# Kernel optimization log

Measured on AMD Instinct MI355X. Metric: run time of the kernel, lower is better.

The kernel has to match this reference:

```python
import jax, jax.numpy as jnp
import numpy as np

N, E, D, H, C = 50000, 800000, 128, 4, 32  # nodes, edges, in/out dim, heads, head dim
NEG_SLOPE = 0.2
LN_EPS = 1e-5
NORM_EPS = 1e-12


def setup_inputs() -> dict:
    key = jax.random.key(0)
    ks = jax.random.split(key, 10)
    s = 1.0 / np.sqrt(D)
    return {
        "x": jax.random.normal(ks[0], (N, D), dtype=jnp.float32),
        "edge_index": jax.random.randint(ks[1], (2, E), 0, N, dtype=jnp.int64),
        "gamma": 1.0 + 0.1 * jax.random.normal(ks[2], (D,), dtype=jnp.float32),
        "beta": 0.1 * jax.random.normal(ks[3], (D,), dtype=jnp.float32),
        "W_l": jax.random.normal(ks[4], (D, H * C), dtype=jnp.float32) * s,
        "b_l": jnp.zeros((H * C,), dtype=jnp.float32),
        "W_r": jax.random.normal(ks[5], (D, H * C), dtype=jnp.float32) * s,
        "b_r": jnp.zeros((H * C,), dtype=jnp.float32),
        "att": jax.random.normal(ks[6], (H, C), dtype=jnp.float32) * s,
        "bias": jnp.zeros((H * C,), dtype=jnp.float32),
        "scale": jnp.array(1.0, dtype=jnp.float32),
    }


def reference(x, edge_index, gamma, beta, W_l, b_l, W_r, b_r, att, bias, scale):
    n = x.shape[0]
    # Pre-activation: LayerNorm -> ReLU (dropout=0 in eval)
    mu = jnp.mean(x, axis=-1, keepdims=True)
    var = jnp.mean(jnp.square(x - mu), axis=-1, keepdims=True)
    h = jax.nn.relu((x - mu) / jnp.sqrt(var + LN_EPS) * gamma + beta)

    # GATv2Conv (PyG defaults: add_self_loops=True, negative_slope=0.2)
    loops = jnp.arange(n, dtype=edge_index.dtype)
    src = jnp.concatenate([edge_index[0], loops])  # message source j
    dst = jnp.concatenate([edge_index[1], loops])  # message target i

    xl = (h @ W_l + b_l).reshape(n, H, C)
    xr = (h @ W_r + b_r).reshape(n, H, C)

    # per-edge GATv2 score: a^T LeakyReLU(xl[j] + xr[i])  -> [E2, H]
    feat = jax.nn.leaky_relu(xl[src] + xr[dst], NEG_SLOPE)
    e = jnp.einsum('ehc,hc->eh', feat, att)

    # segment softmax over incoming edges of each target node
    m = jax.ops.segment_max(e, dst, num_segments=n)
    p = jnp.exp(e - m[dst])
    denom = jax.ops.segment_sum(p, dst, num_segments=n)
    alpha = p / denom[dst]  # [E2, H]

    # scatter-aggregate weighted source features
    msg = alpha[:, :, None] * xl[src]  # [E2, H, C]
    out = jax.ops.segment_sum(msg, dst, num_segments=n).reshape(n, H * C) + bias

    # MsgNorm: normalize(msg) * ||h||_2 * scale
    out_norm = jnp.sqrt(jnp.sum(jnp.square(out), axis=-1, keepdims=True))
    msg_n = out / jnp.maximum(out_norm, NORM_EPS)
    h_norm = jnp.sqrt(jnp.sum(jnp.square(h), axis=-1, keepdims=True))
    gat_out = msg_n * h_norm * scale

    # residual (projection is None since in_channels == out_channels)
    return x + gat_out
```

## Files before the change

### kernel.cpp

```cpp
#include <hip/hip_runtime.h>
#include <hip/hip_bf16.h>
#include <math.h>

#define N_NODES 50000
#define N_EDGES 800000
#define E2 (N_EDGES + N_NODES)
#define D 128

#define NB_LN 12500
#define NB_W 128

#define BSHIFT 8
#define NBUCK 196
#define SCHUNK 4096
#define NB_SC ((E2 + SCHUNK - 1) / SCHUNK)
#define NB_GEMM (((N_NODES + 127) / 128) * 2)

typedef short short8 __attribute__((ext_vector_type(8)));
typedef float f32x4 __attribute__((ext_vector_type(4)));
typedef _Float16 h16x2 __attribute__((ext_vector_type(2)));
typedef _Float16 h16x8 __attribute__((ext_vector_type(8)));

__device__ __forceinline__ float waveReduceSum(float v) {
#pragma unroll
  for (int off = 32; off >= 1; off >>= 1) v += __shfl_xor(v, off);
  return v;
}

__device__ __forceinline__ h16x2 shfl_xor_h2(h16x2 v, int off) {
  int r = __shfl_xor(__builtin_bit_cast(int, v), off);
  return __builtin_bit_cast(h16x2, r);
}

__global__ void __launch_bounds__(256) k_count(const int* __restrict__ ei,
                                               int* __restrict__ bcnt) {
  __shared__ int c[256];
  const int t = threadIdx.x;
  c[t] = 0;
  __syncthreads();
  const int s0 = blockIdx.x * SCHUNK;
#pragma unroll
  for (int k = 0; k < 16; ++k) {
    int e = s0 + t + k * 256;
    if (e < E2) {
      int dst = (e < N_EDGES) ? ei[N_EDGES + e] : (e - N_EDGES);
      atomicAdd(&c[dst >> BSHIFT], 1);
    }
  }
  __syncthreads();
  if (c[t]) atomicAdd(&bcnt[t], c[t]);
}

__global__ void __launch_bounds__(256) k_pre2(
    const float* __restrict__ x, const float* __restrict__ gamma,
    const float* __restrict__ beta, const float* __restrict__ Wl,
    const float* __restrict__ Wr, const int* __restrict__ ei,
    const int* __restrict__ bcnt, int* __restrict__ cnt0,
    int2* __restrict__ bucketed, __hip_bfloat16* __restrict__ hb,
    float* __restrict__ hnorm, __hip_bfloat16* __restrict__ Wt) {
  const int b = blockIdx.x;
  if (b < NB_SC) {
    __shared__ int c[256], base[256], sd[256];
    const int t = threadIdx.x;
    const int own = (t < NBUCK) ? bcnt[t] : 0;
    sd[t] = own;
    c[t] = 0;
    __syncthreads();
    for (int off = 1; off < 256; off <<= 1) {
      int u = 0;
      if (t >= off) u = sd[t - off];
      __syncthreads();
      if (t >= off) sd[t] += u;
      __syncthreads();
    }
    const int boffL = sd[t] - own;
    const int s0 = b * SCHUNK;
#pragma unroll
    for (int k = 0; k < 16; ++k) {
      int e = s0 + t + k * 256;
      if (e < E2) {
        int dst = (e < N_EDGES) ? ei[N_EDGES + e] : (e - N_EDGES);
        atomicAdd(&c[dst >> BSHIFT], 1);
      }
    }
    __syncthreads();
    if (t < NBUCK) {
      base[t] = c[t] ? (boffL + atomicAdd(&cnt0[t], c[t])) : 0;
      c[t] = 0;
    }
    __syncthreads();
#pragma unroll
    for (int k = 0; k < 16; ++k) {
      int e = s0 + t + k * 256;
      if (e < E2) {
        int src, dst;
        if (e < N_EDGES) {
          src = ei[e];
          dst = ei[N_EDGES + e];
        } else {
          src = dst = e - N_EDGES;
        }
        int bk = dst >> BSHIFT;
        int pos = base[bk] + atomicAdd(&c[bk], 1);
        bucketed[pos] = make_int2(src, dst);
      }
    }
  } else if (b < NB_SC + NB_LN) {
    int wid = threadIdx.x >> 6;
    int lane = threadIdx.x & 63;
    int i = (b - NB_SC) * 4 + wid;
    const float2 xv = *(const float2*)&x[(size_t)i * D + lane * 2];
    float s = waveReduceSum(xv.x + xv.y);
    float mean = s * (1.0f / D);
    float d0 = xv.x - mean, d1 = xv.y - mean;
    float vs = waveReduceSum(d0 * d0 + d1 * d1);
    float rstd = rsqrtf(vs * (1.0f / D) + 1e-5f);
    const float2 g = *(const float2*)&gamma[lane * 2];
    const float2 bb = *(const float2*)&beta[lane * 2];
    float h0 = fmaxf(d0 * rstd * g.x + bb.x, 0.0f);
    float h1 = fmaxf(d1 * rstd * g.y + bb.y, 0.0f);
    __hip_bfloat162 hv;
    hv.x = __float2bfloat16(h0);
    hv.y = __float2bfloat16(h1);
    *(__hip_bfloat162*)&hb[(size_t)i * D + lane * 2] = hv;
    float ns = waveReduceSum(h0 * h0 + h1 * h1);
    if (lane == 0) hnorm[i] = sqrtf(ns);
  } else {
    int local = b - NB_SC - NB_LN;
    int n = local * 2 + (threadIdx.x >> 7);
    int k = threadIdx.x & 127;
    float v = (n < D) ? Wl[(size_t)k * D + n] : Wr[(size_t)k * D + (n - D)];
    Wt[n * D + k] = __float2bfloat16(v);
  }
}

__global__ void __launch_bounds__(256) k_mid(
    const int2* __restrict__ bucketed, const int* __restrict__ bcnt,
    int* __restrict__ rowptr, int* __restrict__ csr,
    const __hip_bfloat16* __restrict__ hb, const __hip_bfloat16* __restrict__ Wt,
    const float* __restrict__ bL, const float* __restrict__ bR,
    _Float16* __restrict__ xlh, _Float16* __restrict__ xrh) {
  __shared__ char smem[65536];
  const int t = threadIdx.x;
  if (blockIdx.x < NBUCK) {
    int* cnt = (int*)smem;
    int* tsum = cnt + 256;
    int* cursor = tsum + 256;
    int* red = cursor + 256;
    const int b = blockIdx.x;
    const int base = b << BSHIFT;
    const int nnode = min(256, N_NODES - base);
    red[t] = (t < b) ? bcnt[t] : 0;
    cnt[t] = 0;
    __syncthreads();
    for (int off = 128; off >= 1; off >>= 1) {
      if (t < off) red[t] += red[t + off];
      __syncthreads();
    }
    const int e0 = red[0], e1 = red[0] + bcnt[b];
    if (b == 0) {
      if (t == 0) rowptr[N_NODES] = E2;
      if (t < 32) csr[E2 + t] = 0;
    }
    for (int e = e0 + t; e < e1; e += 256) {
      int2 pr = bucketed[e];
      atomicAdd(&cnt[pr.y - base], 1);
    }
    __syncthreads();
    const int own = cnt[t];
    tsum[t] = own;
    __syncthreads();
    for (int off = 1; off < 256; off <<= 1) {
      int u = 0;
      if (t >= off) u = tsum[t - off];
      __syncthreads();
      if (t >= off) tsum[t] += u;
      __syncthreads();
    }
    const int ebase = e0 + tsum[t] - own;
    cursor[t] = ebase;
    if (t < nnode) rowptr[base + t] = ebase;
    __syncthreads();
    for (int e = e0 + t; e < e1; e += 256) {
      int2 pr = bucketed[e];
      int pos = atomicAdd(&cursor[pr.y - base], 1);
      csr[pos] = pr.x;
    }
  } else {
    unsigned short* As = (unsigned short*)smem;
    unsigned short* Bs = As + 128 * 128;
    const int bid = blockIdx.x - NBUCK;
    const int row0 = (bid >> 1) * 128;
    const int nhalf = bid & 1;
    const unsigned short* hu = (const unsigned short*)hb;
    const unsigned short* wu = (const unsigned short*)Wt;
#pragma unroll
    for (int it = 0; it < 8; ++it) {
      int idx = t + it * 256;
      int r = idx >> 4, g = idx & 15;
      int gs = g ^ (r & 15);
      short8 av = {};
      int grow = row0 + r;
      if (grow < N_NODES) av = *(const short8*)&hu[(size_t)grow * D + g * 8];
      *(short8*)&As[r * 128 + gs * 8] = av;
      short8 bv = *(const short8*)&wu[(size_t)(nhalf * 128 + r) * D + g * 8];
      *(short8*)&Bs[r * 128 + gs * 8] = bv;
    }
    __syncthreads();
    const int w = t >> 6, lane = t & 63;
    const int wm = (w >> 1) * 64, wn = (w & 1) * 64;
    const int lr = lane & 15, lq = lane >> 4;
    f32x4 acc[4][4] = {};
#pragma unroll
    for (int kb = 0; kb < 4; ++kb) {
      short8 af[4], bfr[4];
#pragma unroll
      for (int mi = 0; mi < 4; ++mi) {
        int r = wm + mi * 16 + lr;
        int g = (kb * 4 + lq) ^ (r & 15);
        af[mi] = *(const short8*)&As[r * 128 + g * 8];
      }
#pragma unroll
      for (int ni = 0; ni < 4; ++ni) {
        int r = wn + ni * 16 + lr;
        int g = (kb * 4 + lq) ^ (r & 15);
        bfr[ni] = *(const short8*)&Bs[r * 128 + g * 8];
      }
#pragma unroll
      for (int mi = 0; mi < 4; ++mi)
#pragma unroll
        for (int ni = 0; ni < 4; ++ni)
          acc[mi][ni] = __builtin_amdgcn_mfma_f32_16x16x32_bf16(af[mi], bfr[ni],
                                                                acc[mi][ni], 0, 0, 0);
    }
    const float* bb = (nhalf == 0) ? bL : bR;
    _Float16* dst = (nhalf == 0) ? xlh : xrh;
#pragma unroll
    for (int mi = 0; mi < 4; ++mi) {
#pragma unroll
      for (int ni = 0; ni < 4; ++ni) {
#pragma unroll
        for (int r = 0; r < 4; ++r) {
          int row = row0 + wm + mi * 16 + lq * 4 + r;
          int col = wn + ni * 16 + lr;
          if (row < N_NODES)
            dst[(size_t)row * D + col] = (_Float16)(acc[mi][ni][r] + bb[col]);
        }
      }
    }
  }
}

__global__ void __launch_bounds__(256) k_node(
    const float* __restrict__ x, const _Float16* __restrict__ xlh,
    const _Float16* __restrict__ xrh, const float* __restrict__ hnorm,
    const int* __restrict__ rowptr, const int* __restrict__ csr,
    const float* __restrict__ att, const float* __restrict__ bias,
    const float* __restrict__ scale, float* __restrict__ out) {
  const int wid = threadIdx.x >> 6;
  const int lane = threadIdx.x & 63;
  const int i = blockIdx.x * 4 + wid;
  if (i >= N_NODES) return;
  const int g = lane >> 4;
  const int q = lane & 15;

  const h16x8 xrv = *(const h16x8*)(xrh + (size_t)i * D + q * 8);
  h16x2 xr2[4], at2[4];
  {
    const float LOG2E = 1.44269504f;
    const float4 a0 = *(const float4*)&att[q * 8];
    const float4 a1 = *(const float4*)&att[q * 8 + 4];
    at2[0] = (h16x2){(_Float16)(a0.x * LOG2E), (_Float16)(a0.y * LOG2E)};
    at2[1] = (h16x2){(_Float16)(a0.z * LOG2E), (_Float16)(a0.w * LOG2E)};
    at2[2] = (h16x2){(_Float16)(a1.x * LOG2E), (_Float16)(a1.y * LOG2E)};
    at2[3] = (h16x2){(_Float16)(a1.z * LOG2E), (_Float16)(a1.w * LOG2E)};
#pragma unroll
    for (int z = 0; z < 4; ++z) xr2[z] = (h16x2){xrv[2 * z], xrv[2 * z + 1]};
  }
  const h16x2 c02 = {(_Float16)0.2f, (_Float16)0.2f};

  const int e0 = rowptr[i], e1 = rowptr[i + 1];
  h16x2 A2[4] = {};
  float S = 0.f;

  int ja = csr[e0 + g];
  h16x8 r0 = *(const h16x8*)(xlh + (size_t)ja * D + q * 8);
  int jb = csr[e0 + 4 + g];
  h16x8 r1 = *(const h16x8*)(xlh + (size_t)jb * D + q * 8);
  int jc = csr[e0 + 8 + g];
  h16x8 r2 = *(const h16x8*)(xlh + (size_t)jc * D + q * 8);
  int jd = csr[e0 + 12 + g];

  for (int e = e0; e < e1; e += 4) {
    const h16x8 cur = r0;
    r0 = r1;
    r1 = r2;
    r2 = *(const h16x8*)(xlh + (size_t)jd * D + q * 8);
    jd = csr[e + 16 + g];
    const bool ok = (e + g) < e1;

    h16x2 v2[4];
    v2[0] = (h16x2){cur[0], cur[1]};
    v2[1] = (h16x2){cur[2], cur[3]};
    v2[2] = (h16x2){cur[4], cur[5]};
    v2[3] = (h16x2){cur[6], cur[7]};
    float sc = 0.f;
#pragma unroll
    for (int z = 0; z < 4; ++z) {
      h16x2 f = v2[z] + xr2[z];
      h16x2 lf = __builtin_elementwise_max(f, f * c02);
      sc = __builtin_amdgcn_fdot2(lf, at2[z], sc, false);
    }
    sc += __shfl_xor(sc, 1);
    sc += __shfl_xor(sc, 2);
    const float p = ok ? __builtin_exp2f(sc) : 0.f;
    S += p;
    const _Float16 ph = (_Float16)p;
    const h16x2 p2 = {ph, ph};
#pragma unroll
    for (int z = 0; z < 4; ++z) A2[z] = v2[z] * p2 + A2[z];
  }

#pragma unroll
  for (int off = 16; off <= 32; off <<= 1) {
#pragma unroll
    for (int z = 0; z < 4; ++z) A2[z] = A2[z] + shfl_xor_h2(A2[z], off);
    S += __shfl_xor(S, off);
  }

  const float si = 1.0f / S;
  float o[8];
  float b8[8];
  *(float4*)&b8[0] = *(const float4*)&bias[q * 8];
  *(float4*)&b8[4] = *(const float4*)&bias[q * 8 + 4];
  float dot = 0.f;
#pragma unroll
  for (int z = 0; z < 4; ++z) {
    o[2 * z] = fmaf((float)A2[z][0], si, b8[2 * z]);
    o[2 * z + 1] = fmaf((float)A2[z][1], si, b8[2 * z + 1]);
    dot = fmaf(o[2 * z], o[2 * z], dot);
    dot = fmaf(o[2 * z + 1], o[2 * z + 1], dot);
  }
  const float nrm = sqrtf(waveReduceSum(dot) * 0.25f);
  const float gg = hnorm[i] * scale[0] / fmaxf(nrm, 1e-12f);

  if (lane < 16) {
    float x8[8];
    *(float4*)&x8[0] = *(const float4*)&x[(size_t)i * D + q * 8];
    *(float4*)&x8[4] = *(const float4*)&x[(size_t)i * D + q * 8 + 4];
    float r8[8];
#pragma unroll
    for (int z = 0; z < 8; ++z) r8[z] = fmaf(o[z], gg, x8[z]);
    *(float4*)&out[(size_t)i * D + q * 8] = *(float4*)&r8[0];
    *(float4*)&out[(size_t)i * D + q * 8 + 4] = *(float4*)&r8[4];
  }
}

extern "C" void kernel_launch(void* const* d_in, const int* in_sizes, int n_in,
                              void* d_out, int out_size, void* d_ws, size_t ws_size,
                              hipStream_t stream) {
  const float* x = (const float*)d_in[0];
  const int* ei = (const int*)d_in[1];
  const float* gamma = (const float*)d_in[2];
  const float* beta = (const float*)d_in[3];
  const float* Wl = (const float*)d_in[4];
  const float* bL = (const float*)d_in[5];
  const float* Wr = (const float*)d_in[6];
  const float* bR = (const float*)d_in[7];
  const float* att = (const float*)d_in[8];
  const float* bias = (const float*)d_in[9];
  const float* scale = (const float*)d_in[10];
  float* out = (float*)d_out;

  int2* bucketed = (int2*)d_ws;
  int* csr = (int*)(bucketed + E2);
  int* rowptr = csr + E2 + 32;
  int* bcnt = rowptr + N_NODES + 16;
  int* cnt0 = bcnt + 256;
  float* hnorm = (float*)(cnt0 + 256);
  __hip_bfloat16* hb = (__hip_bfloat16*)(hnorm + N_NODES);
  __hip_bfloat16* Wt = hb + (size_t)N_NODES * D;
  _Float16* xlh = (_Float16*)(Wt + 256 * D);
  _Float16* xrh = xlh + (size_t)N_NODES * D;

  hipMemsetAsync(bcnt, 0, 512 * sizeof(int), stream);
  k_count<<<NB_SC, 256, 0, stream>>>(ei, bcnt);
  k_pre2<<<NB_SC + NB_LN + NB_W, 256, 0, stream>>>(x, gamma, beta, Wl, Wr, ei, bcnt,
                                                   cnt0, bucketed, hb, hnorm, Wt);
  k_mid<<<NBUCK + NB_GEMM, 256, 0, stream>>>(bucketed, bcnt, rowptr, csr, hb, Wt,
                                             bL, bR, xlh, xrh);
  k_node<<<(N_NODES + 3) / 4, 256, 0, stream>>>(x, xlh, xrh, hnorm, rowptr, csr, att,
                                                bias, scale, out);
}
```

Measured before the change: 109.9 us.

## Fuse LayerNorm into GEMM blocks and regroup CSR build stages

LayerNorm+ReLU is now computed directly inside the GEMM blocks and written as bf16 into shared memory, so the intermediate hb buffer is no longer written to or read from global memory. Each GEMM block now covers 128 rows and both the W_l and W_r halves, reusing the normalized A tile and reloading only B. The weight transpose moves into the counting kernel, and bucket scatter runs alongside the GEMM while CSR construction becomes its own kernel. The GEMM blocks become longer and serial (32 rows of LN per wave, then two matmul passes), which cuts parallelism, and the stage ordering changes overlap.

After: 139.5 us. 1.27x slower.

```diff
diff --git a/kernel.cpp b/kernel.cpp
--- a/kernel.cpp
+++ b/kernel.cpp
@@ -7,14 +7,13 @@
 #define E2 (N_EDGES + N_NODES)
 #define D 128
 
-#define NB_LN 12500
 #define NB_W 128
 
 #define BSHIFT 8
 #define NBUCK 196
 #define SCHUNK 4096
 #define NB_SC ((E2 + SCHUNK - 1) / SCHUNK)
-#define NB_GEMM (((N_NODES + 127) / 128) * 2)
+#define NB_G2 ((N_NODES + 127) / 128)
 
 typedef short short8 __attribute__((ext_vector_type(8)));
 typedef float f32x4 __attribute__((ext_vector_type(4)));
@@ -32,36 +31,57 @@
   return __builtin_bit_cast(h16x2, r);
 }
 
-__global__ void __launch_bounds__(256) k_count(const int* __restrict__ ei,
-                                               int* __restrict__ bcnt) {
-  __shared__ int c[256];
-  const int t = threadIdx.x;
-  c[t] = 0;
-  __syncthreads();
-  const int s0 = blockIdx.x * SCHUNK;
-#pragma unroll
-  for (int k = 0; k < 16; ++k) {
-    int e = s0 + t + k * 256;
-    if (e < E2) {
-      int dst = (e < N_EDGES) ? ei[N_EDGES + e] : (e - N_EDGES);
-      atomicAdd(&c[dst >> BSHIFT], 1);
-    }
-  }
-  __syncthreads();
-  if (c[t]) atomicAdd(&bcnt[t], c[t]);
-}
-
-__global__ void __launch_bounds__(256) k_pre2(
-    const float* __restrict__ x, const float* __restrict__ gamma,
-    const float* __restrict__ beta, const float* __restrict__ Wl,
-    const float* __restrict__ Wr, const int* __restrict__ ei,
-    const int* __restrict__ bcnt, int* __restrict__ cnt0,
-    int2* __restrict__ bucketed, __hip_bfloat16* __restrict__ hb,
-    float* __restrict__ hnorm, __hip_bfloat16* __restrict__ Wt) {
+__device__ __forceinline__ unsigned short bf16bits(float f) {
+  unsigned u = __float_as_uint(f);
+  unsigned rounded = u + 0x7fff + ((u >> 16) & 1);
+  return (unsigned short)(rounded >> 16);
+}
+
+__global__ void __launch_bounds__(256) k_pre0(const int* __restrict__ ei,
+                                              const float* __restrict__ Wl,
+                                              const float* __restrict__ Wr,
+                                              __hip_bfloat16* __restrict__ Wt,
+                                              int* __restrict__ bcnt) {
   const int b = blockIdx.x;
   if (b < NB_SC) {
-    __shared__ int c[256], base[256], sd[256];
+    __shared__ int c[256];
     const int t = threadIdx.x;
+    c[t] = 0;
+    __syncthreads();
+    const int s0 = b * SCHUNK;
+#pragma unroll
+    for (int k = 0; k < 16; ++k) {
+      int e = s0 + t + k * 256;
+      if (e < E2) {
+        int dst = (e < N_EDGES) ? ei[N_EDGES + e] : (e - N_EDGES);
+        atomicAdd(&c[dst >> BSHIFT], 1);
+      }
+    }
+    __syncthreads();
+    if (c[t]) atomicAdd(&bcnt[t], c[t]);
+  } else {
+    int local = b - NB_SC;
+    int n = local * 2 + (threadIdx.x >> 7);
+    int k = threadIdx.x & 127;
+    float v = (n < D) ? Wl[(size_t)k * D + n] : Wr[(size_t)k * D + (n - D)];
+    Wt[n * D + k] = __float2bfloat16(v);
+  }
+}
+
+__global__ void __launch_bounds__(256) k_A(
+    const float* __restrict__ x, const float* __restrict__ gamma,
+    const float* __restrict__ beta, const int* __restrict__ ei,
+    const int* __restrict__ bcnt, int* __restrict__ cnt0,
+    int2* __restrict__ bucketed, const __hip_bfloat16* __restrict__ Wt,
+    const float* __restrict__ bL, const float* __restrict__ bR,
+    float* __restrict__ hnorm, _Float16* __restrict__ xlh,
+    _Float16* __restrict__ xrh) {
+  __shared__ char smem[65536];
+  const int t = threadIdx.x;
+  if (blockIdx.x < NB_SC) {
+    int* c = (int*)smem;
+    int* base = c + 256;
+    int* sd = base + 256;
     const int own = (t < NBUCK) ? bcnt[t] : 0;
     sd[t] = own;
     c[t] = 0;
@@ -74,7 +94,7 @@
       __syncthreads();
     }
     const int boffL = sd[t] - own;
-    const int s0 = b * SCHUNK;
+    const int s0 = blockIdx.x * SCHUNK;
 #pragma unroll
     for (int k = 0; k < 16; ++k) {
       int e = s0 + t + k * 256;
@@ -105,149 +125,136 @@
         bucketed[pos] = make_int2(src, dst);
       }
     }
-  } else if (b < NB_SC + NB_LN) {
-    int wid = threadIdx.x >> 6;
-    int lane = threadIdx.x & 63;
-    int i = (b - NB_SC) * 4 + wid;
-    const float2 xv = *(const float2*)&x[(size_t)i * D + lane * 2];
-    float s = waveReduceSum(xv.x + xv.y);
-    float mean = s * (1.0f / D);
-    float d0 = xv.x - mean, d1 = xv.y - mean;
-    float vs = waveReduceSum(d0 * d0 + d1 * d1);
-    float rstd = rsqrtf(vs * (1.0f / D) + 1e-5f);
-    const float2 g = *(const float2*)&gamma[lane * 2];
-    const float2 bb = *(const float2*)&beta[lane * 2];
-    float h0 = fmaxf(d0 * rstd * g.x + bb.x, 0.0f);
-    float h1 = fmaxf(d1 * rstd * g.y + bb.y, 0.0f);
-    __hip_bfloat162 hv;
-    hv.x = __float2bfloat16(h0);
-    hv.y = __float2bfloat16(h1);
-    *(__hip_bfloat162*)&hb[(size_t)i * D + lane * 2] = hv;
-    float ns = waveReduceSum(h0 * h0 + h1 * h1);
-    if (lane == 0) hnorm[i] = sqrtf(ns);
-  } else {
-    int local = b - NB_SC - NB_LN;
-    int n = local * 2 + (threadIdx.x >> 7);
-    int k = threadIdx.x & 127;
-    float v = (n < D) ? Wl[(size_t)k * D + n] : Wr[(size_t)k * D + (n - D)];
-    Wt[n * D + k] = __float2bfloat16(v);
-  }
-}
-
-__global__ void __launch_bounds__(256) k_mid(
-    const int2* __restrict__ bucketed, const int* __restrict__ bcnt,
-    int* __restrict__ rowptr, int* __restrict__ csr,
-    const __hip_bfloat16* __restrict__ hb, const __hip_bfloat16* __restrict__ Wt,
-    const float* __restrict__ bL, const float* __restrict__ bR,
-    _Float16* __restrict__ xlh, _Float16* __restrict__ xrh) {
-  __shared__ char smem[65536];
-  const int t = threadIdx.x;
-  if (blockIdx.x < NBUCK) {
-    int* cnt = (int*)smem;
-    int* tsum = cnt + 256;
-    int* cursor = tsum + 256;
-    int* red = cursor + 256;
-    const int b = blockIdx.x;
-    const int base = b << BSHIFT;
-    const int nnode = min(256, N_NODES - base);
-    red[t] = (t < b) ? bcnt[t] : 0;
-    cnt[t] = 0;
-    __syncthreads();
-    for (int off = 128; off >= 1; off >>= 1) {
-      if (t < off) red[t] += red[t + off];
-      __syncthreads();
-    }
-    const int e0 = red[0], e1 = red[0] + bcnt[b];
-    if (b == 0) {
-      if (t == 0) rowptr[N_NODES] = E2;
-      if (t < 32) csr[E2 + t] = 0;
-    }
-    for (int e = e0 + t; e < e1; e += 256) {
-      int2 pr = bucketed[e];
-      atomicAdd(&cnt[pr.y - base], 1);
-    }
-    __syncthreads();
-    const int own = cnt[t];
-    tsum[t] = own;
-    __syncthreads();
-    for (int off = 1; off < 256; off <<= 1) {
-      int u = 0;
-      if (t >= off) u = tsum[t - off];
-      __syncthreads();
-      if (t >= off) tsum[t] += u;
-      __syncthreads();
-    }
-    const int ebase = e0 + tsum[t] - own;
-    cursor[t] = ebase;
-    if (t < nnode) rowptr[base + t] = ebase;
-    __syncthreads();
-    for (int e = e0 + t; e < e1; e += 256) {
-      int2 pr = bucketed[e];
-      int pos = atomicAdd(&cursor[pr.y - base], 1);
-      csr[pos] = pr.x;
-    }
   } else {
     unsigned short* As = (unsigned short*)smem;
     unsigned short* Bs = As + 128 * 128;
-    const int bid = blockIdx.x - NBUCK;
-    const int row0 = (bid >> 1) * 128;
-    const int nhalf = bid & 1;
-    const unsigned short* hu = (const unsigned short*)hb;
+    const int bid = blockIdx.x - NB_SC;
+    const int row0 = bid * 128;
     const unsigned short* wu = (const unsigned short*)Wt;
-#pragma unroll
-    for (int it = 0; it < 8; ++it) {
-      int idx = t + it * 256;
-      int r = idx >> 4, g = idx & 15;
-      int gs = g ^ (r & 15);
-      short8 av = {};
-      int grow = row0 + r;
-      if (grow < N_NODES) av = *(const short8*)&hu[(size_t)grow * D + g * 8];
-      *(short8*)&As[r * 128 + gs * 8] = av;
-      short8 bv = *(const short8*)&wu[(size_t)(nhalf * 128 + r) * D + g * 8];
-      *(short8*)&Bs[r * 128 + gs * 8] = bv;
-    }
-    __syncthreads();
     const int w = t >> 6, lane = t & 63;
+    {
+      const float2 g2 = *(const float2*)&gamma[lane * 2];
+      const float2 b2 = *(const float2*)&beta[lane * 2];
+      const int gidx0 = lane >> 2;
+      const int goff = (lane * 2) & 7;
+      for (int rr = 0; rr < 32; ++rr) {
+        const int r = (w << 5) + rr;
+        const int grow = row0 + r;
+        float2 xv = make_float2(0.f, 0.f);
+        if (grow < N_NODES) xv = *(const float2*)&x[(size_t)grow * D + lane * 2];
+        float s = waveReduceSum(xv.x + xv.y);
+        float mean = s * (1.0f / D);
+        float d0 = xv.x - mean, d1 = xv.y - mean;
+        float vs = waveReduceSum(d0 * d0 + d1 * d1);
+        float rstd = rsqrtf(vs * (1.0f / D) + 1e-5f);
+        float h0 = fmaxf(d0 * rstd * g2.x + b2.x, 0.0f);
+        float h1 = fmaxf(d1 * rstd * g2.y + b2.y, 0.0f);
+        float ns = waveReduceSum(h0 * h0 + h1 * h1);
+        if (lane == 0 && grow < N_NODES) hnorm[grow] = sqrtf(ns);
+        unsigned pack = (unsigned)bf16bits(h0) | ((unsigned)bf16bits(h1) << 16);
+        *(unsigned*)&As[r * 128 + ((gidx0 ^ (r & 15)) * 8) + goff] = pack;
+      }
+    }
     const int wm = (w >> 1) * 64, wn = (w & 1) * 64;
     const int lr = lane & 15, lq = lane >> 4;
-    f32x4 acc[4][4] = {};
-#pragma unroll
-    for (int kb = 0; kb < 4; ++kb) {
-      short8 af[4], bfr[4];
+#pragma unroll
+    for (int half = 0; half < 2; ++half) {
+      __syncthreads();
+#pragma unroll
+      for (int it = 0; it < 8; ++it) {
+        int idx = t + it * 256;
+        int r = idx >> 4, g = idx & 15;
+        int gs = g ^ (r & 15);
+        short8 bv = *(const short8*)&wu[(size_t)(half * 128 + r) * D + g * 8];
+        *(short8*)&Bs[r * 128 + gs * 8] = bv;
+      }
+      __syncthreads();
+      f32x4 acc[4][4] = {};
+#pragma unroll
+      for (int kb = 0; kb < 4; ++kb) {
+        short8 af[4], bfr[4];
+#pragma unroll
+        for (int mi = 0; mi < 4; ++mi) {
+          int r = wm + mi * 16 + lr;
+          int g = (kb * 4 + lq) ^ (r & 15);
+          af[mi] = *(const short8*)&As[r * 128 + g * 8];
+        }
+#pragma unroll
+        for (int ni = 0; ni < 4; ++ni) {
+          int r = wn + ni * 16 + lr;
+          int g = (kb * 4 + lq) ^ (r & 15);
+          bfr[ni] = *(const short8*)&Bs[r * 128 + g * 8];
+        }
+#pragma unroll
+        for (int mi = 0; mi < 4; ++mi)
+#pragma unroll
+          for (int ni = 0; ni < 4; ++ni)
+            acc[mi][ni] = __builtin_amdgcn_mfma_f32_16x16x32_bf16(af[mi], bfr[ni],
+                                                                  acc[mi][ni], 0, 0, 0);
+      }
+      const float* bb = (half == 0) ? bL : bR;
+      _Float16* dst = (half == 0) ? xlh : xrh;
 #pragma unroll
       for (int mi = 0; mi < 4; ++mi) {
-        int r = wm + mi * 16 + lr;
-        int g = (kb * 4 + lq) ^ (r & 15);
-        af[mi] = *(const short8*)&As[r * 128 + g * 8];
-      }
-#pragma unroll
-      for (int ni = 0; ni < 4; ++ni) {
-        int r = wn + ni * 16 + lr;
-        int g = (kb * 4 + lq) ^ (r & 15);
-        bfr[ni] = *(const short8*)&Bs[r * 128 + g * 8];
-      }
-#pragma unroll
-      for (int mi = 0; mi < 4; ++mi)
-#pragma unroll
-        for (int ni = 0; ni < 4; ++ni)
-          acc[mi][ni] = __builtin_amdgcn_mfma_f32_16x16x32_bf16(af[mi], bfr[ni],
-                                                                acc[mi][ni], 0, 0, 0);
-    }
-    const float* bb = (nhalf == 0) ? bL : bR;
-    _Float16* dst = (nhalf == 0) ? xlh : xrh;
-#pragma unroll
-    for (int mi = 0; mi < 4; ++mi) {
-#pragma unroll
-      for (int ni = 0; ni < 4; ++ni) {
-#pragma unroll
-        for (int r = 0; r < 4; ++r) {
-          int row = row0 + wm + mi * 16 + lq * 4 + r;
-          int col = wn + ni * 16 + lr;
-          if (row < N_NODES)
-            dst[(size_t)row * D + col] = (_Float16)(acc[mi][ni][r] + bb[col]);
+#pragma unroll
+        for (int ni = 0; ni < 4; ++ni) {
+#pragma unroll
+          for (int r = 0; r < 4; ++r) {
+            int row = row0 + wm + mi * 16 + lq * 4 + r;
+            int col = wn + ni * 16 + lr;
+            if (row < N_NODES)
+              dst[(size_t)row * D + col] = (_Float16)(acc[mi][ni][r] + bb[col]);
+          }
         }
       }
     }
+  }
+}
+
+__global__ void __launch_bounds__(256) k_B(const int2* __restrict__ bucketed,
+                                           const int* __restrict__ bcnt,
+                                           int* __restrict__ rowptr,
+                                           int* __restrict__ csr) {
+  __shared__ int cnt[256], tsum[256], cursor[256], red[256];
+  const int b = blockIdx.x;
+  const int base = b << BSHIFT;
+  const int nnode = min(256, N_NODES - base);
+  const int t = threadIdx.x;
+  red[t] = (t < b) ? bcnt[t] : 0;
+  cnt[t] = 0;
+  __syncthreads();
+  for (int off = 128; off >= 1; off >>= 1) {
+    if (t < off) red[t] += red[t + off];
+    __syncthreads();
+  }
+  const int e0 = red[0], e1 = red[0] + bcnt[b];
+  if (b == 0) {
+    if (t == 0) rowptr[N_NODES] = E2;
+    if (t < 32) csr[E2 + t] = 0;
+  }
+  for (int e = e0 + t; e < e1; e += 256) {
+    int2 pr = bucketed[e];
+    atomicAdd(&cnt[pr.y - base], 1);
+  }
+  __syncthreads();
+  const int own = cnt[t];
+  tsum[t] = own;
+  __syncthreads();
+  for (int off = 1; off < 256; off <<= 1) {
+    int u = 0;
+    if (t >= off) u = tsum[t - off];
+    __syncthreads();
+    if (t >= off) tsum[t] += u;
+    __syncthreads();
+  }
+  const int ebase = e0 + tsum[t] - own;
+  cursor[t] = ebase;
+  if (t < nnode) rowptr[base + t] = ebase;
+  __syncthreads();
+  for (int e = e0 + t; e < e1; e += 256) {
+    int2 pr = bucketed[e];
+    int pos = atomicAdd(&cursor[pr.y - base], 1);
+    csr[pos] = pr.x;
   }
 }
 
@@ -378,17 +385,15 @@
   int* bcnt = rowptr + N_NODES + 16;
   int* cnt0 = bcnt + 256;
   float* hnorm = (float*)(cnt0 + 256);
-  __hip_bfloat16* hb = (__hip_bfloat16*)(hnorm + N_NODES);
-  __hip_bfloat16* Wt = hb + (size_t)N_NODES * D;
+  __hip_bfloat16* Wt = (__hip_bfloat16*)(hnorm + N_NODES);
   _Float16* xlh = (_Float16*)(Wt + 256 * D);
   _Float16* xrh = xlh + (size_t)N_NODES * D;
 
-  hipMemsetAsync(bcnt, 0, 512 * sizeof(int), stream);
-  k_count<<<NB_SC, 256, 0, stream>>>(ei, bcnt);
-  k_pre2<<<NB_SC + NB_LN + NB_W, 256, 0, stream>>>(x, gamma, beta, Wl, Wr, ei, bcnt,
-                                                   cnt0, bucketed, hb, hnorm, Wt);
-  k_mid<<<NBUCK + NB_GEMM, 256, 0, stream>>>(bucketed, bcnt, rowptr, csr, hb, Wt,
-                                             bL, bR, xlh, xrh);
+  (void)hipMemsetAsync(bcnt, 0, 512 * sizeof(int), stream);
+  k_pre0<<<NB_SC + NB_W, 256, 0, stream>>>(ei, Wl, Wr, Wt, bcnt);
+  k_A<<<NB_SC + NB_G2, 256, 0, stream>>>(x, gamma, beta, ei, bcnt, cnt0, bucketed,
+                                         Wt, bL, bR, hnorm, xlh, xrh);
+  k_B<<<NBUCK, 256, 0, stream>>>(bucketed, bcnt, rowptr, csr);
   k_node<<<(N_NODES + 3) / 4, 256, 0, stream>>>(x, xlh, xrh, hnorm, rowptr, csr, att,
                                                 bias, scale, out);
 }
```
